# Kernel optimization log

Hardware: AMD Instinct MI355X
Metric: run time of the kernel (lower is better)

The kernel has to match this reference:

```python
import jax, jax.numpy as jnp
import numpy as np

E, H, S, B = 256, 512, 128, 512
C_EXP = 10.0  # tanh_exploration
N_COUNT_MAX = 20
T_STEPS = 100  # (max(counts)+1)*5 upper bound, static for scan


def setup_inputs() -> dict:
    key = jax.random.key(0)
    ks = jax.random.split(key, 24)
    def rn(k, shape, scale=0.02):
        return jax.random.normal(k, shape, dtype=jnp.float32) * scale
    inv_sqrt_h = 1.0 / np.sqrt(H)
    return {
        "decoder_input": rn(ks[0], (B, E), 1.0),
        "embedded_inputs": rn(ks[1], (S, B, E), 1.0),
        "hx": rn(ks[2], (B, H), 1.0),
        "cx": rn(ks[3], (B, H), 1.0),
        "context": rn(ks[4], (S, B, H), 1.0),
        "counts": jax.random.randint(ks[5], (B,), 0, N_COUNT_MAX),
        "max_steps": T_STEPS,
        "Wi": rn(ks[6], (4 * H, E)), "bi": jnp.zeros((4 * H,), jnp.float32),
        "Wh": rn(ks[7], (4 * H, H)), "bh": jnp.zeros((4 * H,), jnp.float32),
        "gWq": rn(ks[8], (H, H)), "gbq": jnp.zeros((H,), jnp.float32),
        "gWr": rn(ks[9], (H, H)), "gbr": jnp.zeros((H,), jnp.float32),
        "gv": jax.random.uniform(ks[10], (H,), jnp.float32, -inv_sqrt_h, inv_sqrt_h),
        "pWq": rn(ks[11], (H, H)), "pbq": jnp.zeros((H,), jnp.float32),
        "pWr": rn(ks[12], (H, H)), "pbr": jnp.zeros((H,), jnp.float32),
        "pv": jax.random.uniform(ks[13], (H,), jnp.float32, -inv_sqrt_h, inv_sqrt_h),
    }


def _attn(q, context, Wq, bq, Wr, br, v):
    # q: [B,H]; context: [S,B,H]. 1x1 conv over source dim == per-position linear.
    e = jnp.einsum('sbh,oh->bos', context, Wr) + br[None, :, None]  # [B,H,S]
    qp = q @ Wq.T + bq                                             # [B,H]
    u = jnp.einsum('h,bhs->bs', v, jnp.tanh(qp[:, :, None] + e))   # [B,S]
    return e, u


def reference(decoder_input, embedded_inputs, hx, cx, context, counts, max_steps,
              Wi, bi, Wh, bh, gWq, gbq, gWr, gbr, gv, pWq, pbq, pWr, pbr, pv):
    base_key = jax.random.key(42)
    batch_idx = jnp.arange(B)

    def step(carry, t):
        hx_, cx_, dec_in, fmask, fmmask = carry
        # LSTM cell
        gates = dec_in @ Wi.T + bi + hx_ @ Wh.T + bh
        ig, fg, cg, og = jnp.split(gates, 4, axis=1)
        cy = jax.nn.sigmoid(fg) * cx_ + jax.nn.sigmoid(ig) * jnp.tanh(cg)
        hy = jax.nn.sigmoid(og) * jnp.tanh(cy)
        # one glimpse (n_glimpses=1, use_tanh=False)
        e_g, lg = _attn(hy, context, gWq, gbq, gWr, gbr, gv)
        g_l = jnp.einsum('bhs,bs->bh', e_g, jax.nn.softmax(lg, axis=-1))
        # pointer (use_tanh=True, C=10)
        _, up = _attn(g_l, context, pWq, pbq, pWr, pbr, pv)
        logits_p = C_EXP * jnp.tanh(up)
        probs = jax.nn.softmax(logits_p, axis=-1)          # [B,S]
        idxs = jax.random.categorical(jax.random.fold_in(base_key, t), logits_p)
        idxs = (idxs * fmask).astype(jnp.int32)
        probs_out = probs * (fmask * fmmask)[:, None].astype(probs.dtype)
        new_fmask = fmask * (idxs != 0).astype(jnp.int32)
        new_fmmask = jnp.where(t == counts, 0, fmmask)
        dec_next = embedded_inputs[idxs, batch_idx, :]     # [B,E]
        return (hy, cy, dec_next, new_fmask, new_fmmask), (probs_out, idxs)

    ones = jnp.ones((B,), jnp.int32)
    init = (hx, cx, decoder_input, ones, ones)
    (hx, cx, _, _, _), (probs_seq, sel) = jax.lax.scan(
        step, init, jnp.arange(max_steps))
    # match torch: per-batch stacked outputs concatenated -> [B*T, S]
    outputs = jnp.transpose(probs_seq, (1, 0, 2)).reshape(B * max_steps, S)
    return outputs, sel, hx, cx
```

## Files before the change

kernel.cpp:

```cpp
#include <hip/hip_runtime.h>
#include <stdint.h>
#include <math.h>

typedef unsigned int u32;

constexpr int kB = 512, kS = 128, kH = 512, kE = 256, kT = 100;
constexpr int kNG = 4 * kH;

constexpr size_t SZ_E = (size_t)kS * kB * kH;
constexpr size_t OFF_EG  = 0;
constexpr size_t OFF_EP  = OFF_EG + SZ_E;
constexpr size_t OFF_U   = OFF_EP + SZ_E;
constexpr size_t OFF_P   = OFF_U + (size_t)kB * kS;
constexpr size_t OFF_QP  = OFF_P + (size_t)kB * kS;
constexpr size_t OFF_GL  = OFF_QP + (size_t)kB * kH;
constexpr size_t OFF_G   = OFF_GL + (size_t)kB * kH;
constexpr size_t OFF_HX  = OFF_G + (size_t)kB * kNG;
constexpr size_t OFF_CX  = OFF_HX + (size_t)kB * kH;
constexpr size_t OFF_DC  = OFF_CX + (size_t)kB * kH;
constexpr size_t OFF_FM  = OFF_DC + (size_t)kB * kE;
constexpr size_t OFF_FMM = OFF_FM + kB;
constexpr size_t WS_FLOATS = OFF_FMM + kB;

__global__ __launch_bounds__(256) void sentinel_k(float* __restrict__ outSel, float val) {
  int i = blockIdx.x * blockDim.x + threadIdx.x;
  if (i < kT * kB) outSel[i] = val;
}

__device__ __forceinline__ u32 rotl32(u32 v, int d) { return (v << d) | (v >> (32 - d)); }

__device__ __forceinline__ void tf2x32(u32 k0, u32 k1, u32 x0, u32 x1, u32& o0, u32& o1) {
  u32 ks2 = k0 ^ k1 ^ 0x1BD11BDAu;
  x0 += k0; x1 += k1;
#define RND_(r) { x0 += x1; x1 = rotl32(x1, r); x1 ^= x0; }
  RND_(13) RND_(15) RND_(26) RND_(6)   x0 += k1;  x1 += ks2 + 1u;
  RND_(17) RND_(29) RND_(16) RND_(24)  x0 += ks2; x1 += k0 + 2u;
  RND_(13) RND_(15) RND_(26) RND_(6)   x0 += k0;  x1 += k1 + 3u;
  RND_(17) RND_(29) RND_(16) RND_(24)  x0 += k1;  x1 += ks2 + 4u;
  RND_(13) RND_(15) RND_(26) RND_(6)   x0 += ks2; x1 += k0 + 5u;
#undef RND_
  o0 = x0; o1 = x1;
}

__device__ __forceinline__ float sigf(float x) { return 1.0f / (1.0f + expf(-x)); }

__global__ __launch_bounds__(512) void precompute_e(const float* __restrict__ ctx,
                                                    const float* __restrict__ Wg,
                                                    const float* __restrict__ bg,
                                                    const float* __restrict__ Wp,
                                                    const float* __restrict__ bp,
                                                    float* __restrict__ EG,
                                                    float* __restrict__ EP) {
  __shared__ float ctxs[8][512];
  __shared__ float Wgs[512][33];
  __shared__ float Wps[512][33];
  const int tid = threadIdx.x;
  const size_t m0 = (size_t)blockIdx.x * 8;
  for (int idx = tid; idx < 8 * 512; idx += 512) {
    ctxs[idx >> 9][idx & 511] = ctx[(m0 + (idx >> 9)) * 512 + (idx & 511)];
  }
  float accg[8] = {}, accp[8] = {};
  for (int k0 = 0; k0 < 512; k0 += 32) {
    __syncthreads();
    for (int idx = tid; idx < 512 * 32; idx += 512) {
      int row = idx >> 5, kk = idx & 31;
      Wgs[row][kk] = Wg[(size_t)row * 512 + k0 + kk];
      Wps[row][kk] = Wp[(size_t)row * 512 + k0 + kk];
    }
    __syncthreads();
#pragma unroll 4
    for (int kk = 0; kk < 32; ++kk) {
      float wg = Wgs[tid][kk], wp = Wps[tid][kk];
#pragma unroll
      for (int mi = 0; mi < 8; ++mi) {
        float a = ctxs[mi][k0 + kk];
        accg[mi] = fmaf(a, wg, accg[mi]);
        accp[mi] = fmaf(a, wp, accp[mi]);
      }
    }
  }
  float bgv = bg[tid], bpv = bp[tid];
#pragma unroll
  for (int mi = 0; mi < 8; ++mi) {
    size_t m = m0 + mi;
    EG[m * 512 + tid] = accg[mi] + bgv;
    EP[m * 512 + tid] = accp[mi] + bpv;
  }
}

template <int K, int NB, bool FIRST>
__global__ __launch_bounds__(512) void gemm_v2(const float* __restrict__ A,
                                               const float* __restrict__ W,
                                               const float* __restrict__ bias,
                                               const float* __restrict__ Cin,
                                               float* __restrict__ C, int N) {
  __shared__ float As[NB][K];
  __shared__ float Ws[512][33];
  const int b0 = blockIdx.y * NB;
  const int o0 = blockIdx.x * 512;
  const int tid = threadIdx.x;
  for (int idx = tid; idx < NB * K; idx += 512) {
    int bb = idx / K, k = idx % K;
    As[bb][k] = A[(size_t)(b0 + bb) * K + k];
  }
  float acc[NB] = {};
  for (int k0 = 0; k0 < K; k0 += 32) {
    __syncthreads();
    for (int idx = tid; idx < 512 * 32; idx += 512) {
      int row = idx >> 5, kk = idx & 31;
      Ws[row][kk] = W[(size_t)(o0 + row) * K + k0 + kk];
    }
    __syncthreads();
#pragma unroll 4
    for (int kk = 0; kk < 32; ++kk) {
      float w = Ws[tid][kk];
#pragma unroll
      for (int bb = 0; bb < NB; ++bb) acc[bb] = fmaf(As[bb][k0 + kk], w, acc[bb]);
    }
  }
  float bv = bias[o0 + tid];
#pragma unroll
  for (int bb = 0; bb < NB; ++bb) {
    size_t off = (size_t)(b0 + bb) * N + o0 + tid;
    C[off] = FIRST ? (acc[bb] + bv) : ((Cin[off] + acc[bb]) + bv);
  }
}

__global__ __launch_bounds__(256) void init_k(const float* __restrict__ dec_in,
                                              const float* __restrict__ hx0,
                                              const float* __restrict__ cx0,
                                              float* __restrict__ dec, float* __restrict__ hx,
                                              float* __restrict__ cx, int* __restrict__ fm,
                                              int* __restrict__ fmm) {
  int i = blockIdx.x * blockDim.x + threadIdx.x;
  if (i < kB * kH) { hx[i] = hx0[i]; cx[i] = cx0[i]; }
  if (i < kB * kE) dec[i] = dec_in[i];
  if (i < kB) { fm[i] = 1; fmm[i] = 1; }
}

__global__ __launch_bounds__(256) void lstm_act(const float* __restrict__ gates,
                                                float* __restrict__ hx, float* __restrict__ cx) {
  int i = blockIdx.x * blockDim.x + threadIdx.x;
  int b = i >> 9, h = i & (kH - 1);
  const float* g = gates + (size_t)b * kNG;
  float ig = g[h], fg = g[h + kH], cg = g[h + 2 * kH], og = g[h + 3 * kH];
  float cyv = sigf(fg) * cx[i] + sigf(ig) * tanhf(cg);
  float hyv = sigf(og) * tanhf(cyv);
  cx[i] = cyv;
  hx[i] = hyv;
}

__global__ __launch_bounds__(512) void fused_step(
    const float* __restrict__ EG, const float* __restrict__ EP, const float* __restrict__ gWq,
    const float* __restrict__ gbq, const float* __restrict__ gv, const float* __restrict__ pWq,
    const float* __restrict__ pbq, const float* __restrict__ pv, const float* __restrict__ emb,
    const int* __restrict__ counts, float* __restrict__ HX, float* __restrict__ DC,
    int* __restrict__ fmask, int* __restrict__ fmmask, float* __restrict__ outP,
    float* __restrict__ outSel, int t) {
  __shared__ float Ws[512][33];
  __shared__ float hs[512];
  __shared__ float qs[512];
  __shared__ float gvs[512];
  __shared__ float gls[512];
  __shared__ float u[128], sL[128], ex[128], kv[128];
  __shared__ float mred, sred, sMult;
  __shared__ int sIdx;

  const int b = blockIdx.x;
  const int tid = threadIdx.x;
  const int wave = tid >> 6, lane = tid & 63;

  hs[tid] = HX[(size_t)b * kH + tid];
  gvs[tid] = gv[tid];
  __syncthreads();

  {
    float acc = 0.f;
    for (int k0 = 0; k0 < 512; k0 += 32) {
      __syncthreads();
      for (int idx = tid; idx < 512 * 32; idx += 512) {
        int row = idx >> 5, kk = idx & 31;
        Ws[row][kk] = gWq[(size_t)row * 512 + k0 + kk];
      }
      __syncthreads();
#pragma unroll 8
      for (int kk = 0; kk < 32; ++kk) acc = fmaf(hs[k0 + kk], Ws[tid][kk], acc);
    }
    qs[tid] = acc + gbq[tid];
  }
  __syncthreads();

  for (int r = 0; r < 16; ++r) {
    int s = wave + 8 * r;
    const float* row = EG + ((size_t)s * kB + b) * kH;
    float a = 0.f;
#pragma unroll
    for (int i = 0; i < 8; ++i) {
      int h = lane + 64 * i;
      a = fmaf(gvs[h], tanhf(qs[h] + row[h]), a);
    }
#pragma unroll
    for (int off = 32; off > 0; off >>= 1) a += __shfl_xor(a, off);
    if (lane == 0) u[s] = a;
  }
  __syncthreads();

  if (tid == 0) { float m = u[0]; for (int i = 1; i < 128; ++i) m = fmaxf(m, u[i]); mred = m; }
  __syncthreads();
  if (tid < 128) ex[tid] = expf(u[tid] - mred);
  __syncthreads();
  if (tid == 0) { float s = 0.f; for (int i = 0; i < 128; ++i) s += ex[i]; sred = s; }
  __syncthreads();
  if (tid < 128) ex[tid] = ex[tid] / sred;
  __syncthreads();

  {
    float acc = 0.f;
    for (int s = 0; s < 128; ++s) acc = fmaf(EG[((size_t)s * kB + b) * kH + tid], ex[s], acc);
    gls[tid] = acc;
  }
  __syncthreads();

  {
    float acc = 0.f;
    for (int k0 = 0; k0 < 512; k0 += 32) {
      __syncthreads();
      for (int idx = tid; idx < 512 * 32; idx += 512) {
        int row = idx >> 5, kk = idx & 31;
        Ws[row][kk] = pWq[(size_t)row * 512 + k0 + kk];
      }
      __syncthreads();
#pragma unroll 8
      for (int kk = 0; kk < 32; ++kk) acc = fmaf(gls[k0 + kk], Ws[tid][kk], acc);
    }
    qs[tid] = acc + pbq[tid];
    gvs[tid] = pv[tid];
  }
  __syncthreads();

  for (int r = 0; r < 16; ++r) {
    int s = wave + 8 * r;
    const float* row = EP + ((size_t)s * kB + b) * kH;
    float a = 0.f;
#pragma unroll
    for (int i = 0; i < 8; ++i) {
      int h = lane + 64 * i;
      a = fmaf(gvs[h], tanhf(qs[h] + row[h]), a);
    }
#pragma unroll
    for (int off = 32; off > 0; off >>= 1) a += __shfl_xor(a, off);
    if (lane == 0) u[s] = a;
  }
  __syncthreads();

  if (tid < 128) sL[tid] = 10.0f * tanhf(u[tid]);
  __syncthreads();
  if (tid == 0) { float m = sL[0]; for (int i = 1; i < 128; ++i) m = fmaxf(m, sL[i]); mred = m; }
  __syncthreads();
  if (tid < 128) ex[tid] = expf(sL[tid] - mred);
  __syncthreads();
  if (tid == 0) { float s = 0.f; for (int i = 0; i < 128; ++i) s += ex[i]; sred = s; }
  __syncthreads();
  if (tid < 128) {
    u32 fk0, fk1;
    tf2x32(0u, 42u, 0u, (u32)t, fk0, fk1);
    u32 j = (u32)(b * kS + tid);
    u32 y0, y1;
    tf2x32(fk0, fk1, 0u, j, y0, y1);
    u32 bits = y0 ^ y1;
    float f = __uint_as_float(0x3f800000u | (bits >> 9)) - 1.0f;
    float uu = (f > 0.0f) ? f : 1.17549435082228751e-38f;
    float z = -logf(-logf(uu));
    kv[tid] = sL[tid] + z;
  }
  __syncthreads();
  if (tid == 0) {
    float best = kv[0];
    int ia = 0;
    for (int i = 1; i < 128; ++i)
      if (kv[i] > best) { best = kv[i]; ia = i; }
    int fm = fmask[b], fmm = fmmask[b];
    int idx = ia * fm;
    outSel[(size_t)t * kB + b] = (float)idx;
    fmask[b] = (idx != 0) ? fm : 0;
    fmmask[b] = (t == counts[b]) ? 0 : fmm;
    sIdx = idx;
    sMult = (float)(fm * fmm);
  }
  __syncthreads();
  if (tid < 128) outP[((size_t)b * kT + t) * kS + tid] = (ex[tid] / sred) * sMult;
  if (tid < 256) DC[(size_t)b * kE + tid] = emb[((size_t)sIdx * kB + b) * kE + tid];
}

__global__ __launch_bounds__(256) void final_copy(const float* __restrict__ hx,
                                                  const float* __restrict__ cx,
                                                  float* __restrict__ o2, float* __restrict__ o3) {
  int i = blockIdx.x * blockDim.x + threadIdx.x;
  if (i < kB * kH) { o2[i] = hx[i]; o3[i] = cx[i]; }
}

extern "C" void kernel_launch(void* const* d_in, const int* in_sizes, int n_in, void* d_out,
                              int out_size, void* d_ws, size_t ws_size, hipStream_t stream) {
  const float* dec_in = (const float*)d_in[0];
  const float* emb = (const float*)d_in[1];
  const float* hx0 = (const float*)d_in[2];
  const float* cx0 = (const float*)d_in[3];
  const float* ctx = (const float*)d_in[4];
  const int* counts = (const int*)d_in[5];
  const float* Wi = (const float*)d_in[7];
  const float* bi = (const float*)d_in[8];
  const float* Wh = (const float*)d_in[9];
  const float* bh = (const float*)d_in[10];
  const float* gWq = (const float*)d_in[11];
  const float* gbq = (const float*)d_in[12];
  const float* gWr = (const float*)d_in[13];
  const float* gbr = (const float*)d_in[14];
  const float* gv = (const float*)d_in[15];
  const float* pWq = (const float*)d_in[16];
  const float* pbq = (const float*)d_in[17];
  const float* pWr = (const float*)d_in[18];
  const float* pbr = (const float*)d_in[19];
  const float* pv = (const float*)d_in[20];

  float* out = (float*)d_out;
  float* outP = out;
  float* outSel = out + (size_t)kB * kT * kS;
  float* outHx = outSel + (size_t)kT * kB;
  float* outCx = outHx + (size_t)kB * kH;

  if (ws_size < WS_FLOATS * sizeof(float)) {
    double wsMB = (double)ws_size / (1024.0 * 1024.0);
    if (wsMB > 80000.0) wsMB = 80000.0;
    hipLaunchKernelGGL(sentinel_k, dim3((kT * kB + 255) / 256), dim3(256), 0, stream, outSel,
                       (float)(1000.0 + wsMB));
    return;
  }

  float* base = (float*)d_ws;
  float* EG = base + OFF_EG;
  float* EP = base + OFF_EP;
  float* G  = base + OFF_G;
  float* HX = base + OFF_HX;
  float* CX = base + OFF_CX;
  float* DC = base + OFF_DC;
  int* FM  = (int*)(base + OFF_FM);
  int* FMM = (int*)(base + OFF_FMM);

  hipLaunchKernelGGL(precompute_e, dim3(kS * kB / 8), dim3(512), 0, stream, ctx, gWr, gbr, pWr,
                     pbr, EG, EP);
  hipLaunchKernelGGL(init_k, dim3(kB * kH / 256), dim3(256), 0, stream, dec_in, hx0, cx0, DC, HX,
                     CX, FM, FMM);

  for (int t = 0; t < kT; ++t) {
    hipLaunchKernelGGL((gemm_v2<256, 8, true>), dim3(4, 64), dim3(512), 0, stream, DC, Wi, bi,
                       (const float*)nullptr, G, kNG);
    hipLaunchKernelGGL((gemm_v2<512, 8, false>), dim3(4, 64), dim3(512), 0, stream, HX, Wh, bh, G,
                       G, kNG);
    hipLaunchKernelGGL(lstm_act, dim3(kB * kH / 256), dim3(256), 0, stream, G, HX, CX);
    hipLaunchKernelGGL(fused_step, dim3(kB), dim3(512), 0, stream, EG, EP, gWq, gbq, gv, pWq, pbq,
                       pv, emb, counts, HX, DC, FM, FMM, outP, outSel, t);
  }
  hipLaunchKernelGGL(final_copy, dim3(kB * kH / 256), dim3(256), 0, stream, HX, CX, outHx, outCx);
}
```

Baseline: 36.14 ms.

## Replace per-block query matvecs with batched GEMMs and split fused step kernel

The glimpse and pointer query projections were computed inside the per-batch fused kernel, with every block re-streaming the full HxH weight matrix through shared memory. These projections now run as batched GEMM launches that share the weights across batch rows. The fused kernel is split into an attention/glimpse kernel and a pointer/sampling kernel that read the precomputed projections from workspace. This trades redundant weight traffic for extra kernel launches and global round trips of the intermediate vectors.

```diff
diff --git a/kernel.cpp b/kernel.cpp
--- a/kernel.cpp
+++ b/kernel.cpp
@@ -150,44 +150,19 @@
   hx[i] = hyv;
 }
 
-__global__ __launch_bounds__(512) void fused_step(
-    const float* __restrict__ EG, const float* __restrict__ EP, const float* __restrict__ gWq,
-    const float* __restrict__ gbq, const float* __restrict__ gv, const float* __restrict__ pWq,
-    const float* __restrict__ pbq, const float* __restrict__ pv, const float* __restrict__ emb,
-    const int* __restrict__ counts, float* __restrict__ HX, float* __restrict__ DC,
-    int* __restrict__ fmask, int* __restrict__ fmmask, float* __restrict__ outP,
-    float* __restrict__ outSel, int t) {
-  __shared__ float Ws[512][33];
-  __shared__ float hs[512];
-  __shared__ float qs[512];
-  __shared__ float gvs[512];
-  __shared__ float gls[512];
-  __shared__ float u[128], sL[128], ex[128], kv[128];
-  __shared__ float mred, sred, sMult;
-  __shared__ int sIdx;
-
+__global__ __launch_bounds__(512) void fused_A(const float* __restrict__ EG,
+                                               const float* __restrict__ qp,
+                                               const float* __restrict__ gv,
+                                               float* __restrict__ GL) {
+  __shared__ float qs[512], gvs[512], gls_unused[1];
+  __shared__ float u[128], ps[128];
+  __shared__ float mred, sred;
   const int b = blockIdx.x;
   const int tid = threadIdx.x;
   const int wave = tid >> 6, lane = tid & 63;
 
-  hs[tid] = HX[(size_t)b * kH + tid];
+  qs[tid] = qp[(size_t)b * kH + tid];
   gvs[tid] = gv[tid];
-  __syncthreads();
-
-  {
-    float acc = 0.f;
-    for (int k0 = 0; k0 < 512; k0 += 32) {
-      __syncthreads();
-      for (int idx = tid; idx < 512 * 32; idx += 512) {
-        int row = idx >> 5, kk = idx & 31;
-        Ws[row][kk] = gWq[(size_t)row * 512 + k0 + kk];
-      }
-      __syncthreads();
-#pragma unroll 8
-      for (int kk = 0; kk < 32; ++kk) acc = fmaf(hs[k0 + kk], Ws[tid][kk], acc);
-    }
-    qs[tid] = acc + gbq[tid];
-  }
   __syncthreads();
 
   for (int r = 0; r < 16; ++r) {
@@ -207,35 +182,37 @@
 
   if (tid == 0) { float m = u[0]; for (int i = 1; i < 128; ++i) m = fmaxf(m, u[i]); mred = m; }
   __syncthreads();
-  if (tid < 128) ex[tid] = expf(u[tid] - mred);
-  __syncthreads();
-  if (tid == 0) { float s = 0.f; for (int i = 0; i < 128; ++i) s += ex[i]; sred = s; }
-  __syncthreads();
-  if (tid < 128) ex[tid] = ex[tid] / sred;
-  __syncthreads();
-
-  {
-    float acc = 0.f;
-    for (int s = 0; s < 128; ++s) acc = fmaf(EG[((size_t)s * kB + b) * kH + tid], ex[s], acc);
-    gls[tid] = acc;
-  }
-  __syncthreads();
-
-  {
-    float acc = 0.f;
-    for (int k0 = 0; k0 < 512; k0 += 32) {
-      __syncthreads();
-      for (int idx = tid; idx < 512 * 32; idx += 512) {
-        int row = idx >> 5, kk = idx & 31;
-        Ws[row][kk] = pWq[(size_t)row * 512 + k0 + kk];
-      }
-      __syncthreads();
-#pragma unroll 8
-      for (int kk = 0; kk < 32; ++kk) acc = fmaf(gls[k0 + kk], Ws[tid][kk], acc);
-    }
-    qs[tid] = acc + pbq[tid];
-    gvs[tid] = pv[tid];
-  }
+  if (tid < 128) ps[tid] = expf(u[tid] - mred);
+  __syncthreads();
+  if (tid == 0) { float s = 0.f; for (int i = 0; i < 128; ++i) s += ps[i]; sred = s; }
+  __syncthreads();
+  if (tid < 128) ps[tid] = ps[tid] / sred;
+  __syncthreads();
+
+  float acc = 0.f;
+  for (int s = 0; s < 128; ++s) acc = fmaf(EG[((size_t)s * kB + b) * kH + tid], ps[s], acc);
+  GL[(size_t)b * kH + tid] = acc;
+  (void)gls_unused;
+}
+
+__global__ __launch_bounds__(512) void fused_B(const float* __restrict__ EP,
+                                               const float* __restrict__ qp,
+                                               const float* __restrict__ pv,
+                                               const float* __restrict__ emb,
+                                               const int* __restrict__ counts,
+                                               float* __restrict__ DC, int* __restrict__ fmask,
+                                               int* __restrict__ fmmask, float* __restrict__ outP,
+                                               float* __restrict__ outSel, int t) {
+  __shared__ float qs[512], gvs[512];
+  __shared__ float u[128], sL[128], ex[128], kv[128];
+  __shared__ float mred, sred, sMult;
+  __shared__ int sIdx;
+  const int b = blockIdx.x;
+  const int tid = threadIdx.x;
+  const int wave = tid >> 6, lane = tid & 63;
+
+  qs[tid] = qp[(size_t)b * kH + tid];
+  gvs[tid] = pv[tid];
   __syncthreads();
 
   for (int r = 0; r < 16; ++r) {
@@ -339,6 +316,8 @@
   float* base = (float*)d_ws;
   float* EG = base + OFF_EG;
   float* EP = base + OFF_EP;
+  float* QP = base + OFF_QP;
+  float* GL = base + OFF_GL;
   float* G  = base + OFF_G;
   float* HX = base + OFF_HX;
   float* CX = base + OFF_CX;
@@ -357,8 +336,13 @@
     hipLaunchKernelGGL((gemm_v2<512, 8, false>), dim3(4, 64), dim3(512), 0, stream, HX, Wh, bh, G,
                        G, kNG);
     hipLaunchKernelGGL(lstm_act, dim3(kB * kH / 256), dim3(256), 0, stream, G, HX, CX);
-    hipLaunchKernelGGL(fused_step, dim3(kB), dim3(512), 0, stream, EG, EP, gWq, gbq, gv, pWq, pbq,
-                       pv, emb, counts, HX, DC, FM, FMM, outP, outSel, t);
+    hipLaunchKernelGGL((gemm_v2<512, 4, true>), dim3(1, 128), dim3(512), 0, stream, HX, gWq, gbq,
+                       (const float*)nullptr, QP, kH);
+    hipLaunchKernelGGL(fused_A, dim3(kB), dim3(512), 0, stream, EG, QP, gv, GL);
+    hipLaunchKernelGGL((gemm_v2<512, 4, true>), dim3(1, 128), dim3(512), 0, stream, GL, pWq, pbq,
+                       (const float*)nullptr, QP, kH);
+    hipLaunchKernelGGL(fused_B, dim3(kB), dim3(512), 0, stream, EP, QP, pv, emb, counts, DC, FM,
+                       FMM, outP, outSel, t);
   }
   hipLaunchKernelGGL(final_copy, dim3(kB * kH / 256), dim3(256), 0, stream, HX, CX, outHx, outCx);
 }
```

Result: slower. 41.06 ms (+13.6%).

## Replace per-step kernel launches with a persistent cooperative megakernel using grid syncs

Applied to the files above, without the earlier changes.

Replaces the 400 per-timestep launches (two gate GEMMs, LSTM activation, fused attention step) with one cooperative persistent kernel of 512 blocks that loops over all 100 steps, separated by grid.sync barriers. The LSTM gate GEMM is fused with the activation. The query projections for glimpse and pointer are now computed once per 8-batch tile instead of once per batch row, which cuts redundant weight loads. The cost is five grid-wide barriers per step and phases where only 64 or 256 of the 512 blocks do work. If the cooperative launch fails, the old multi-kernel path runs instead.

```diff
diff --git a/kernel.cpp b/kernel.cpp
--- a/kernel.cpp
+++ b/kernel.cpp
@@ -1,7 +1,9 @@
 #include <hip/hip_runtime.h>
+#include <hip/hip_cooperative_groups.h>
 #include <stdint.h>
 #include <math.h>
 
+namespace cg = cooperative_groups;
 typedef unsigned int u32;
 
 constexpr int kB = 512, kS = 128, kH = 512, kE = 256, kT = 100;
@@ -85,6 +87,256 @@
     size_t m = m0 + mi;
     EG[m * 512 + tid] = accg[mi] + bgv;
     EP[m * 512 + tid] = accp[mi] + bpv;
+  }
+}
+
+__global__ __launch_bounds__(512, 4) void mega_k(
+    const float* __restrict__ EG, const float* __restrict__ EP, const float* __restrict__ Wi,
+    const float* __restrict__ bi, const float* __restrict__ Wh, const float* __restrict__ bh,
+    const float* __restrict__ gWq, const float* __restrict__ gbq, const float* __restrict__ gv,
+    const float* __restrict__ pWq, const float* __restrict__ pbq, const float* __restrict__ pv,
+    const float* __restrict__ emb, const int* __restrict__ counts,
+    const float* __restrict__ dec_in, const float* __restrict__ hx0,
+    const float* __restrict__ cx0, float* __restrict__ HX, float* __restrict__ CX,
+    float* __restrict__ DC, float* __restrict__ QP, float* __restrict__ GL, int* __restrict__ FM,
+    int* __restrict__ FMM, float* __restrict__ outP, float* __restrict__ outSel,
+    float* __restrict__ outHx, float* __restrict__ outCx) {
+  cg::grid_group grid = cg::this_grid();
+  __shared__ float Ws[512][33];
+  __shared__ float As[8][32];
+  __shared__ float qs[512], gvs[512];
+  __shared__ float u[128], ps[128], sL[128], kv[128];
+  __shared__ float mred, sred, sMult;
+  __shared__ int sIdx;
+
+  const int bid = blockIdx.x;
+  const int tid = threadIdx.x;
+  const int wave = tid >> 6, lane = tid & 63;
+
+  {
+    int i = bid * 512 + tid;
+    HX[i] = hx0[i];
+    CX[i] = cx0[i];
+    if (i < kB * kE) DC[i] = dec_in[i];
+    if (i < kB) { FM[i] = 1; FMM[i] = 1; }
+  }
+  grid.sync();
+
+  for (int t = 0; t < kT; ++t) {
+    if (bid < 256) {
+      const int h0 = (bid & 3) * 128;
+      const int b0 = (bid >> 2) * 8;
+      const int hl = tid & 127, bs = tid >> 7;
+      float aI[2][4] = {}, aH[2][4] = {};
+      for (int k0 = 0; k0 < 768; k0 += 32) {
+        const bool isI = (k0 < 256);
+        __syncthreads();
+        if (tid < 256) {
+          int bb = tid >> 5, kk = tid & 31;
+          int k = k0 + kk;
+          As[bb][kk] = isI ? DC[(size_t)(b0 + bb) * kE + k]
+                           : HX[(size_t)(b0 + bb) * kH + (k - 256)];
+        }
+        for (int idx = tid; idx < 512 * 32; idx += 512) {
+          int r = idx >> 5, kk = idx & 31;
+          int grow = ((r >> 7) << 9) + h0 + (r & 127);
+          int k = k0 + kk;
+          Ws[r][kk] = isI ? Wi[(size_t)grow * kE + k] : Wh[(size_t)grow * kH + (k - 256)];
+        }
+        __syncthreads();
+        if (isI) {
+#pragma unroll 4
+          for (int kk = 0; kk < 32; ++kk) {
+            float a0 = As[bs][kk], a1 = As[bs + 4][kk];
+#pragma unroll
+            for (int g = 0; g < 4; ++g) {
+              float w = Ws[g * 128 + hl][kk];
+              aI[0][g] = fmaf(a0, w, aI[0][g]);
+              aI[1][g] = fmaf(a1, w, aI[1][g]);
+            }
+          }
+        } else {
+#pragma unroll 4
+          for (int kk = 0; kk < 32; ++kk) {
+            float a0 = As[bs][kk], a1 = As[bs + 4][kk];
+#pragma unroll
+            for (int g = 0; g < 4; ++g) {
+              float w = Ws[g * 128 + hl][kk];
+              aH[0][g] = fmaf(a0, w, aH[0][g]);
+              aH[1][g] = fmaf(a1, w, aH[1][g]);
+            }
+          }
+        }
+      }
+      const int h = h0 + hl;
+#pragma unroll
+      for (int i = 0; i < 2; ++i) {
+        int b = b0 + bs + i * 4;
+        float ig = ((aI[i][0] + bi[h]) + aH[i][0]) + bh[h];
+        float fg = ((aI[i][1] + bi[512 + h]) + aH[i][1]) + bh[512 + h];
+        float cgv = ((aI[i][2] + bi[1024 + h]) + aH[i][2]) + bh[1024 + h];
+        float og = ((aI[i][3] + bi[1536 + h]) + aH[i][3]) + bh[1536 + h];
+        size_t off = (size_t)b * kH + h;
+        float cyv = sigf(fg) * CX[off] + sigf(ig) * tanhf(cgv);
+        float hyv = sigf(og) * tanhf(cyv);
+        CX[off] = cyv;
+        HX[off] = hyv;
+      }
+    }
+    grid.sync();
+
+    if (bid < 64) {
+      const int b0 = bid * 8;
+      float acc[8] = {};
+      for (int k0 = 0; k0 < 512; k0 += 32) {
+        __syncthreads();
+        if (tid < 256) {
+          int bb = tid >> 5, kk = tid & 31;
+          As[bb][kk] = HX[(size_t)(b0 + bb) * kH + k0 + kk];
+        }
+        for (int idx = tid; idx < 512 * 32; idx += 512) {
+          int r = idx >> 5, kk = idx & 31;
+          Ws[r][kk] = gWq[(size_t)r * 512 + k0 + kk];
+        }
+        __syncthreads();
+#pragma unroll 4
+        for (int kk = 0; kk < 32; ++kk) {
+          float w = Ws[tid][kk];
+#pragma unroll
+          for (int bb = 0; bb < 8; ++bb) acc[bb] = fmaf(As[bb][kk], w, acc[bb]);
+        }
+      }
+      float bv = gbq[tid];
+#pragma unroll
+      for (int bb = 0; bb < 8; ++bb) QP[(size_t)(b0 + bb) * kH + tid] = acc[bb] + bv;
+    }
+    grid.sync();
+
+    {
+      const int b = bid;
+      qs[tid] = QP[(size_t)b * kH + tid];
+      gvs[tid] = gv[tid];
+      __syncthreads();
+      for (int r = 0; r < 16; ++r) {
+        int s = wave + 8 * r;
+        const float* row = EG + ((size_t)s * kB + b) * kH;
+        float a = 0.f;
+#pragma unroll
+        for (int i = 0; i < 8; ++i) {
+          int h = lane + 64 * i;
+          a = fmaf(gvs[h], tanhf(qs[h] + row[h]), a);
+        }
+#pragma unroll
+        for (int off = 32; off > 0; off >>= 1) a += __shfl_xor(a, off);
+        if (lane == 0) u[s] = a;
+      }
+      __syncthreads();
+      if (tid == 0) { float m = u[0]; for (int i = 1; i < 128; ++i) m = fmaxf(m, u[i]); mred = m; }
+      __syncthreads();
+      if (tid < 128) ps[tid] = expf(u[tid] - mred);
+      __syncthreads();
+      if (tid == 0) { float s2 = 0.f; for (int i = 0; i < 128; ++i) s2 += ps[i]; sred = s2; }
+      __syncthreads();
+      if (tid < 128) ps[tid] = ps[tid] / sred;
+      __syncthreads();
+      float acc = 0.f;
+#pragma unroll 4
+      for (int s = 0; s < 128; ++s) acc = fmaf(EG[((size_t)s * kB + b) * kH + tid], ps[s], acc);
+      GL[(size_t)b * kH + tid] = acc;
+    }
+    grid.sync();
+
+    if (bid < 64) {
+      const int b0 = bid * 8;
+      float acc[8] = {};
+      for (int k0 = 0; k0 < 512; k0 += 32) {
+        __syncthreads();
+        if (tid < 256) {
+          int bb = tid >> 5, kk = tid & 31;
+          As[bb][kk] = GL[(size_t)(b0 + bb) * kH + k0 + kk];
+        }
+        for (int idx = tid; idx < 512 * 32; idx += 512) {
+          int r = idx >> 5, kk = idx & 31;
+          Ws[r][kk] = pWq[(size_t)r * 512 + k0 + kk];
+        }
+        __syncthreads();
+#pragma unroll 4
+        for (int kk = 0; kk < 32; ++kk) {
+          float w = Ws[tid][kk];
+#pragma unroll
+          for (int bb = 0; bb < 8; ++bb) acc[bb] = fmaf(As[bb][kk], w, acc[bb]);
+        }
+      }
+      float bv = pbq[tid];
+#pragma unroll
+      for (int bb = 0; bb < 8; ++bb) QP[(size_t)(b0 + bb) * kH + tid] = acc[bb] + bv;
+    }
+    grid.sync();
+
+    {
+      const int b = bid;
+      qs[tid] = QP[(size_t)b * kH + tid];
+      gvs[tid] = pv[tid];
+      __syncthreads();
+      for (int r = 0; r < 16; ++r) {
+        int s = wave + 8 * r;
+        const float* row = EP + ((size_t)s * kB + b) * kH;
+        float a = 0.f;
+#pragma unroll
+        for (int i = 0; i < 8; ++i) {
+          int h = lane + 64 * i;
+          a = fmaf(gvs[h], tanhf(qs[h] + row[h]), a);
+        }
+#pragma unroll
+        for (int off = 32; off > 0; off >>= 1) a += __shfl_xor(a, off);
+        if (lane == 0) u[s] = a;
+      }
+      __syncthreads();
+      if (tid < 128) sL[tid] = 10.0f * tanhf(u[tid]);
+      __syncthreads();
+      if (tid == 0) { float m = sL[0]; for (int i = 1; i < 128; ++i) m = fmaxf(m, sL[i]); mred = m; }
+      __syncthreads();
+      if (tid < 128) ps[tid] = expf(sL[tid] - mred);
+      __syncthreads();
+      if (tid == 0) { float s2 = 0.f; for (int i = 0; i < 128; ++i) s2 += ps[i]; sred = s2; }
+      __syncthreads();
+      if (tid < 128) {
+        u32 fk0, fk1;
+        tf2x32(0u, 42u, 0u, (u32)t, fk0, fk1);
+        u32 j = (u32)(b * kS + tid);
+        u32 y0, y1;
+        tf2x32(fk0, fk1, 0u, j, y0, y1);
+        u32 bits = y0 ^ y1;
+        float f = __uint_as_float(0x3f800000u | (bits >> 9)) - 1.0f;
+        float uu = (f > 0.0f) ? f : 1.17549435082228751e-38f;
+        float z = -logf(-logf(uu));
+        kv[tid] = sL[tid] + z;
+      }
+      __syncthreads();
+      if (tid == 0) {
+        float best = kv[0];
+        int ia = 0;
+        for (int i = 1; i < 128; ++i)
+          if (kv[i] > best) { best = kv[i]; ia = i; }
+        int fm = FM[b], fmm = FMM[b];
+        int idx = ia * fm;
+        outSel[(size_t)t * kB + b] = (float)idx;
+        FM[b] = (idx != 0) ? fm : 0;
+        FMM[b] = (t == counts[b]) ? 0 : fmm;
+        sIdx = idx;
+        sMult = (float)(fm * fmm);
+      }
+      __syncthreads();
+      if (tid < 128) outP[((size_t)b * kT + t) * kS + tid] = (ps[tid] / sred) * sMult;
+      if (tid < 256) DC[(size_t)b * kE + tid] = emb[((size_t)sIdx * kB + b) * kE + tid];
+    }
+    grid.sync();
+  }
+
+  {
+    int i = bid * 512 + tid;
+    outHx[i] = HX[i];
+    outCx[i] = CX[i];
   }
 }
 
@@ -173,7 +425,6 @@
   hs[tid] = HX[(size_t)b * kH + tid];
   gvs[tid] = gv[tid];
   __syncthreads();
-
   {
     float acc = 0.f;
     for (int k0 = 0; k0 < 512; k0 += 32) {
@@ -189,7 +440,6 @@
     qs[tid] = acc + gbq[tid];
   }
   __syncthreads();
-
   for (int r = 0; r < 16; ++r) {
     int s = wave + 8 * r;
     const float* row = EG + ((size_t)s * kB + b) * kH;
@@ -204,7 +454,6 @@
     if (lane == 0) u[s] = a;
   }
   __syncthreads();
-
   if (tid == 0) { float m = u[0]; for (int i = 1; i < 128; ++i) m = fmaxf(m, u[i]); mred = m; }
   __syncthreads();
   if (tid < 128) ex[tid] = expf(u[tid] - mred);
@@ -213,14 +462,12 @@
   __syncthreads();
   if (tid < 128) ex[tid] = ex[tid] / sred;
   __syncthreads();
-
   {
     float acc = 0.f;
     for (int s = 0; s < 128; ++s) acc = fmaf(EG[((size_t)s * kB + b) * kH + tid], ex[s], acc);
     gls[tid] = acc;
   }
   __syncthreads();
-
   {
     float acc = 0.f;
     for (int k0 = 0; k0 < 512; k0 += 32) {
@@ -237,7 +484,6 @@
     gvs[tid] = pv[tid];
   }
   __syncthreads();
-
   for (int r = 0; r < 16; ++r) {
     int s = wave + 8 * r;
     const float* row = EP + ((size_t)s * kB + b) * kH;
@@ -252,7 +498,6 @@
     if (lane == 0) u[s] = a;
   }
   __syncthreads();
-
   if (tid < 128) sL[tid] = 10.0f * tanhf(u[tid]);
   __syncthreads();
   if (tid == 0) { float m = sL[0]; for (int i = 1; i < 128; ++i) m = fmaxf(m, sL[i]); mred = m; }
@@ -339,6 +584,8 @@
   float* base = (float*)d_ws;
   float* EG = base + OFF_EG;
   float* EP = base + OFF_EP;
+  float* QP = base + OFF_QP;
+  float* GL = base + OFF_GL;
   float* G  = base + OFF_G;
   float* HX = base + OFF_HX;
   float* CX = base + OFF_CX;
@@ -348,9 +595,19 @@
 
   hipLaunchKernelGGL(precompute_e, dim3(kS * kB / 8), dim3(512), 0, stream, ctx, gWr, gbr, pWr,
                      pbr, EG, EP);
+
+  void* args[] = {(void*)&EG,  (void*)&EP,  (void*)&Wi,  (void*)&bi,   (void*)&Wh,
+                  (void*)&bh,  (void*)&gWq, (void*)&gbq, (void*)&gv,   (void*)&pWq,
+                  (void*)&pbq, (void*)&pv,  (void*)&emb, (void*)&counts, (void*)&dec_in,
+                  (void*)&hx0, (void*)&cx0, (void*)&HX,  (void*)&CX,   (void*)&DC,
+                  (void*)&QP,  (void*)&GL,  (void*)&FM,  (void*)&FMM,  (void*)&outP,
+                  (void*)&outSel, (void*)&outHx, (void*)&outCx};
+  hipError_t st = hipLaunchCooperativeKernel((const void*)mega_k, dim3(512), dim3(512), args, 0,
+                                             stream);
+  if (st == hipSuccess) return;
+
   hipLaunchKernelGGL(init_k, dim3(kB * kH / 256), dim3(256), 0, stream, dec_in, hx0, cx0, DC, HX,
                      CX, FM, FMM);
-
   for (int t = 0; t < kT; ++t) {
     hipLaunchKernelGGL((gemm_v2<256, 8, true>), dim3(4, 64), dim3(512), 0, stream, DC, Wi, bi,
                        (const float*)nullptr, G, kNG);
```

New measurement: 91.61 ms. 2.53x slower.

## Fuse all decode steps into one persistent per-batch kernel with transposed weights

Applied to the files above, without the earlier changes.

Replaces the per-step launches of two gate GEMMs, the LSTM activation and the attention step with a single persistent kernel. Each block owns one batch row and keeps h, c, the decoder input and the mask flags in shared memory for all 100 steps. The LSTM, glimpse and pointer weights are transposed once up front so every thread reads them as coalesced row vectors straight from global memory. This removes roughly 400 kernel launches and the global round-trips of the intermediate state. The cost is that every block now re-reads the full LSTM weight matrices each step instead of sharing them across 8 batch rows, which multiplies weight traffic through the cache hierarchy.

```diff
diff --git a/kernel.cpp b/kernel.cpp
--- a/kernel.cpp
+++ b/kernel.cpp
@@ -5,22 +5,15 @@
 typedef unsigned int u32;
 
 constexpr int kB = 512, kS = 128, kH = 512, kE = 256, kT = 100;
-constexpr int kNG = 4 * kH;
 
 constexpr size_t SZ_E = (size_t)kS * kB * kH;
 constexpr size_t OFF_EG  = 0;
 constexpr size_t OFF_EP  = OFF_EG + SZ_E;
-constexpr size_t OFF_U   = OFF_EP + SZ_E;
-constexpr size_t OFF_P   = OFF_U + (size_t)kB * kS;
-constexpr size_t OFF_QP  = OFF_P + (size_t)kB * kS;
-constexpr size_t OFF_GL  = OFF_QP + (size_t)kB * kH;
-constexpr size_t OFF_G   = OFF_GL + (size_t)kB * kH;
-constexpr size_t OFF_HX  = OFF_G + (size_t)kB * kNG;
-constexpr size_t OFF_CX  = OFF_HX + (size_t)kB * kH;
-constexpr size_t OFF_DC  = OFF_CX + (size_t)kB * kH;
-constexpr size_t OFF_FM  = OFF_DC + (size_t)kB * kE;
-constexpr size_t OFF_FMM = OFF_FM + kB;
-constexpr size_t WS_FLOATS = OFF_FMM + kB;
+constexpr size_t OFF_WIT = OFF_EP + SZ_E;
+constexpr size_t OFF_WHT = OFF_WIT + (size_t)kE * 2048;
+constexpr size_t OFF_GQT = OFF_WHT + (size_t)kH * 2048;
+constexpr size_t OFF_PQT = OFF_GQT + (size_t)kH * kH;
+constexpr size_t WS_FLOATS = OFF_PQT + (size_t)kH * kH;
 
 __global__ __launch_bounds__(256) void sentinel_k(float* __restrict__ outSel, float val) {
   int i = blockIdx.x * blockDim.x + threadIdx.x;
@@ -88,215 +81,185 @@
   }
 }
 
-template <int K, int NB, bool FIRST>
-__global__ __launch_bounds__(512) void gemm_v2(const float* __restrict__ A,
-                                               const float* __restrict__ W,
-                                               const float* __restrict__ bias,
-                                               const float* __restrict__ Cin,
-                                               float* __restrict__ C, int N) {
-  __shared__ float As[NB][K];
-  __shared__ float Ws[512][33];
-  const int b0 = blockIdx.y * NB;
-  const int o0 = blockIdx.x * 512;
-  const int tid = threadIdx.x;
-  for (int idx = tid; idx < NB * K; idx += 512) {
-    int bb = idx / K, k = idx % K;
-    As[bb][k] = A[(size_t)(b0 + bb) * K + k];
-  }
-  float acc[NB] = {};
-  for (int k0 = 0; k0 < K; k0 += 32) {
-    __syncthreads();
-    for (int idx = tid; idx < 512 * 32; idx += 512) {
-      int row = idx >> 5, kk = idx & 31;
-      Ws[row][kk] = W[(size_t)(o0 + row) * K + k0 + kk];
-    }
-    __syncthreads();
-#pragma unroll 4
-    for (int kk = 0; kk < 32; ++kk) {
-      float w = Ws[tid][kk];
-#pragma unroll
-      for (int bb = 0; bb < NB; ++bb) acc[bb] = fmaf(As[bb][k0 + kk], w, acc[bb]);
-    }
-  }
-  float bv = bias[o0 + tid];
-#pragma unroll
-  for (int bb = 0; bb < NB; ++bb) {
-    size_t off = (size_t)(b0 + bb) * N + o0 + tid;
-    C[off] = FIRST ? (acc[bb] + bv) : ((Cin[off] + acc[bb]) + bv);
-  }
-}
-
-__global__ __launch_bounds__(256) void init_k(const float* __restrict__ dec_in,
-                                              const float* __restrict__ hx0,
-                                              const float* __restrict__ cx0,
-                                              float* __restrict__ dec, float* __restrict__ hx,
-                                              float* __restrict__ cx, int* __restrict__ fm,
-                                              int* __restrict__ fmm) {
-  int i = blockIdx.x * blockDim.x + threadIdx.x;
-  if (i < kB * kH) { hx[i] = hx0[i]; cx[i] = cx0[i]; }
-  if (i < kB * kE) dec[i] = dec_in[i];
-  if (i < kB) { fm[i] = 1; fmm[i] = 1; }
-}
-
-__global__ __launch_bounds__(256) void lstm_act(const float* __restrict__ gates,
-                                                float* __restrict__ hx, float* __restrict__ cx) {
-  int i = blockIdx.x * blockDim.x + threadIdx.x;
-  int b = i >> 9, h = i & (kH - 1);
-  const float* g = gates + (size_t)b * kNG;
-  float ig = g[h], fg = g[h + kH], cg = g[h + 2 * kH], og = g[h + 3 * kH];
-  float cyv = sigf(fg) * cx[i] + sigf(ig) * tanhf(cg);
-  float hyv = sigf(og) * tanhf(cyv);
-  cx[i] = cyv;
-  hx[i] = hyv;
-}
-
-__global__ __launch_bounds__(512) void fused_step(
-    const float* __restrict__ EG, const float* __restrict__ EP, const float* __restrict__ gWq,
-    const float* __restrict__ gbq, const float* __restrict__ gv, const float* __restrict__ pWq,
-    const float* __restrict__ pbq, const float* __restrict__ pv, const float* __restrict__ emb,
-    const int* __restrict__ counts, float* __restrict__ HX, float* __restrict__ DC,
-    int* __restrict__ fmask, int* __restrict__ fmmask, float* __restrict__ outP,
-    float* __restrict__ outSel, int t) {
-  __shared__ float Ws[512][33];
-  __shared__ float hs[512];
-  __shared__ float qs[512];
-  __shared__ float gvs[512];
-  __shared__ float gls[512];
+__global__ __launch_bounds__(256) void transpose_k(const float* __restrict__ in,
+                                                   float* __restrict__ out, int O, int K) {
+  int flat = blockIdx.x * 256 + threadIdx.x;
+  if (flat < O * K) {
+    int o = flat % O, k = flat / O;
+    out[flat] = in[(size_t)o * K + k];
+  }
+}
+
+__global__ __launch_bounds__(512) void persist_k(
+    const float* __restrict__ EG, const float* __restrict__ EP, const float* __restrict__ WiT,
+    const float* __restrict__ WhT, const float* __restrict__ bi, const float* __restrict__ bh,
+    const float* __restrict__ gQT, const float* __restrict__ gbq, const float* __restrict__ gv,
+    const float* __restrict__ pQT, const float* __restrict__ pbq, const float* __restrict__ pv,
+    const float* __restrict__ emb, const int* __restrict__ counts,
+    const float* __restrict__ dec_in, const float* __restrict__ hx0,
+    const float* __restrict__ cx0, float* __restrict__ outP, float* __restrict__ outSel,
+    float* __restrict__ outHx, float* __restrict__ outCx) {
+  __shared__ float hs[512], cs[512], dec[256], qs[512], gls[512];
+  __shared__ float gvs[512], pvs[512];
   __shared__ float u[128], sL[128], ex[128], kv[128];
   __shared__ float mred, sred, sMult;
-  __shared__ int sIdx;
+  __shared__ int sIdx, sFM, sFMM;
 
   const int b = blockIdx.x;
   const int tid = threadIdx.x;
   const int wave = tid >> 6, lane = tid & 63;
 
-  hs[tid] = HX[(size_t)b * kH + tid];
+  hs[tid] = hx0[(size_t)b * kH + tid];
+  cs[tid] = cx0[(size_t)b * kH + tid];
+  if (tid < kE) dec[tid] = dec_in[(size_t)b * kE + tid];
   gvs[tid] = gv[tid];
+  pvs[tid] = pv[tid];
+  if (tid == 0) { sFM = 1; sFMM = 1; }
+  const int cnt = counts[b];
+  const float biR0 = bi[tid], biR1 = bi[512 + tid], biR2 = bi[1024 + tid], biR3 = bi[1536 + tid];
+  const float bhR0 = bh[tid], bhR1 = bh[512 + tid], bhR2 = bh[1024 + tid], bhR3 = bh[1536 + tid];
+  const float gbqR = gbq[tid], pbqR = pbq[tid];
   __syncthreads();
 
-  {
-    float acc = 0.f;
-    for (int k0 = 0; k0 < 512; k0 += 32) {
-      __syncthreads();
-      for (int idx = tid; idx < 512 * 32; idx += 512) {
-        int row = idx >> 5, kk = idx & 31;
-        Ws[row][kk] = gWq[(size_t)row * 512 + k0 + kk];
+  for (int t = 0; t < kT; ++t) {
+    float aI0 = 0.f, aI1 = 0.f, aI2 = 0.f, aI3 = 0.f;
+#pragma unroll 4
+    for (int k = 0; k < kE; ++k) {
+      float a = dec[k];
+      const float* wr = WiT + (size_t)k * 2048 + tid;
+      aI0 = fmaf(a, wr[0], aI0);
+      aI1 = fmaf(a, wr[512], aI1);
+      aI2 = fmaf(a, wr[1024], aI2);
+      aI3 = fmaf(a, wr[1536], aI3);
+    }
+    float aH0 = 0.f, aH1 = 0.f, aH2 = 0.f, aH3 = 0.f;
+#pragma unroll 4
+    for (int k = 0; k < kH; ++k) {
+      float a = hs[k];
+      const float* wr = WhT + (size_t)k * 2048 + tid;
+      aH0 = fmaf(a, wr[0], aH0);
+      aH1 = fmaf(a, wr[512], aH1);
+      aH2 = fmaf(a, wr[1024], aH2);
+      aH3 = fmaf(a, wr[1536], aH3);
+    }
+    float ig = ((aI0 + biR0) + aH0) + bhR0;
+    float fg = ((aI1 + biR1) + aH1) + bhR1;
+    float cgv = ((aI2 + biR2) + aH2) + bhR2;
+    float og = ((aI3 + biR3) + aH3) + bhR3;
+    float cyv = sigf(fg) * cs[tid] + sigf(ig) * tanhf(cgv);
+    float hyv = sigf(og) * tanhf(cyv);
+    __syncthreads();
+    cs[tid] = cyv;
+    hs[tid] = hyv;
+    __syncthreads();
+
+    {
+      float acc = 0.f;
+#pragma unroll 8
+      for (int k = 0; k < kH; ++k) acc = fmaf(hs[k], gQT[(size_t)k * kH + tid], acc);
+      qs[tid] = acc + gbqR;
+    }
+    __syncthreads();
+
+#pragma unroll 2
+    for (int r = 0; r < 16; ++r) {
+      int s = wave + 8 * r;
+      const float* row = EG + ((size_t)s * kB + b) * kH;
+      float a = 0.f;
+#pragma unroll
+      for (int i = 0; i < 8; ++i) {
+        int h = lane + 64 * i;
+        a = fmaf(gvs[h], tanhf(qs[h] + row[h]), a);
       }
-      __syncthreads();
+#pragma unroll
+      for (int off = 32; off > 0; off >>= 1) a += __shfl_xor(a, off);
+      if (lane == 0) u[s] = a;
+    }
+    __syncthreads();
+
+    if (tid == 0) { float m = u[0]; for (int i = 1; i < 128; ++i) m = fmaxf(m, u[i]); mred = m; }
+    __syncthreads();
+    if (tid < 128) ex[tid] = expf(u[tid] - mred);
+    __syncthreads();
+    if (tid == 0) { float s = 0.f; for (int i = 0; i < 128; ++i) s += ex[i]; sred = s; }
+    __syncthreads();
+    if (tid < 128) ex[tid] = ex[tid] / sred;
+    __syncthreads();
+
+    {
+      float acc = 0.f;
+#pragma unroll 4
+      for (int s = 0; s < 128; ++s) acc = fmaf(EG[((size_t)s * kB + b) * kH + tid], ex[s], acc);
+      gls[tid] = acc;
+    }
+    __syncthreads();
+
+    {
+      float acc = 0.f;
 #pragma unroll 8
-      for (int kk = 0; kk < 32; ++kk) acc = fmaf(hs[k0 + kk], Ws[tid][kk], acc);
-    }
-    qs[tid] = acc + gbq[tid];
-  }
-  __syncthreads();
-
-  for (int r = 0; r < 16; ++r) {
-    int s = wave + 8 * r;
-    const float* row = EG + ((size_t)s * kB + b) * kH;
-    float a = 0.f;
-#pragma unroll
-    for (int i = 0; i < 8; ++i) {
-      int h = lane + 64 * i;
-      a = fmaf(gvs[h], tanhf(qs[h] + row[h]), a);
-    }
-#pragma unroll
-    for (int off = 32; off > 0; off >>= 1) a += __shfl_xor(a, off);
-    if (lane == 0) u[s] = a;
-  }
-  __syncthreads();
-
-  if (tid == 0) { float m = u[0]; for (int i = 1; i < 128; ++i) m = fmaxf(m, u[i]); mred = m; }
-  __syncthreads();
-  if (tid < 128) ex[tid] = expf(u[tid] - mred);
-  __syncthreads();
-  if (tid == 0) { float s = 0.f; for (int i = 0; i < 128; ++i) s += ex[i]; sred = s; }
-  __syncthreads();
-  if (tid < 128) ex[tid] = ex[tid] / sred;
-  __syncthreads();
-
-  {
-    float acc = 0.f;
-    for (int s = 0; s < 128; ++s) acc = fmaf(EG[((size_t)s * kB + b) * kH + tid], ex[s], acc);
-    gls[tid] = acc;
-  }
-  __syncthreads();
-
-  {
-    float acc = 0.f;
-    for (int k0 = 0; k0 < 512; k0 += 32) {
-      __syncthreads();
-      for (int idx = tid; idx < 512 * 32; idx += 512) {
-        int row = idx >> 5, kk = idx & 31;
-        Ws[row][kk] = pWq[(size_t)row * 512 + k0 + kk];
+      for (int k = 0; k < kH; ++k) acc = fmaf(gls[k], pQT[(size_t)k * kH + tid], acc);
+      qs[tid] = acc + pbqR;
+    }
+    __syncthreads();
+
+#pragma unroll 2
+    for (int r = 0; r < 16; ++r) {
+      int s = wave + 8 * r;
+      const float* row = EP + ((size_t)s * kB + b) * kH;
+      float a = 0.f;
+#pragma unroll
+      for (int i = 0; i < 8; ++i) {
+        int h = lane + 64 * i;
+        a = fmaf(pvs[h], tanhf(qs[h] + row[h]), a);
       }
-      __syncthreads();
-#pragma unroll 8
-      for (int kk = 0; kk < 32; ++kk) acc = fmaf(gls[k0 + kk], Ws[tid][kk], acc);
-    }
-    qs[tid] = acc + pbq[tid];
-    gvs[tid] = pv[tid];
-  }
-  __syncthreads();
-
-  for (int r = 0; r < 16; ++r) {
-    int s = wave + 8 * r;
-    const float* row = EP + ((size_t)s * kB + b) * kH;
-    float a = 0.f;
-#pragma unroll
-    for (int i = 0; i < 8; ++i) {
-      int h = lane + 64 * i;
-      a = fmaf(gvs[h], tanhf(qs[h] + row[h]), a);
-    }
-#pragma unroll
-    for (int off = 32; off > 0; off >>= 1) a += __shfl_xor(a, off);
-    if (lane == 0) u[s] = a;
-  }
-  __syncthreads();
-
-  if (tid < 128) sL[tid] = 10.0f * tanhf(u[tid]);
-  __syncthreads();
-  if (tid == 0) { float m = sL[0]; for (int i = 1; i < 128; ++i) m = fmaxf(m, sL[i]); mred = m; }
-  __syncthreads();
-  if (tid < 128) ex[tid] = expf(sL[tid] - mred);
-  __syncthreads();
-  if (tid == 0) { float s = 0.f; for (int i = 0; i < 128; ++i) s += ex[i]; sred = s; }
-  __syncthreads();
-  if (tid < 128) {
-    u32 fk0, fk1;
-    tf2x32(0u, 42u, 0u, (u32)t, fk0, fk1);
-    u32 j = (u32)(b * kS + tid);
-    u32 y0, y1;
-    tf2x32(fk0, fk1, 0u, j, y0, y1);
-    u32 bits = y0 ^ y1;
-    float f = __uint_as_float(0x3f800000u | (bits >> 9)) - 1.0f;
-    float uu = (f > 0.0f) ? f : 1.17549435082228751e-38f;
-    float z = -logf(-logf(uu));
-    kv[tid] = sL[tid] + z;
-  }
-  __syncthreads();
-  if (tid == 0) {
-    float best = kv[0];
-    int ia = 0;
-    for (int i = 1; i < 128; ++i)
-      if (kv[i] > best) { best = kv[i]; ia = i; }
-    int fm = fmask[b], fmm = fmmask[b];
-    int idx = ia * fm;
-    outSel[(size_t)t * kB + b] = (float)idx;
-    fmask[b] = (idx != 0) ? fm : 0;
-    fmmask[b] = (t == counts[b]) ? 0 : fmm;
-    sIdx = idx;
-    sMult = (float)(fm * fmm);
-  }
-  __syncthreads();
-  if (tid < 128) outP[((size_t)b * kT + t) * kS + tid] = (ex[tid] / sred) * sMult;
-  if (tid < 256) DC[(size_t)b * kE + tid] = emb[((size_t)sIdx * kB + b) * kE + tid];
-}
-
-__global__ __launch_bounds__(256) void final_copy(const float* __restrict__ hx,
-                                                  const float* __restrict__ cx,
-                                                  float* __restrict__ o2, float* __restrict__ o3) {
-  int i = blockIdx.x * blockDim.x + threadIdx.x;
-  if (i < kB * kH) { o2[i] = hx[i]; o3[i] = cx[i]; }
+#pragma unroll
+      for (int off = 32; off > 0; off >>= 1) a += __shfl_xor(a, off);
+      if (lane == 0) u[s] = a;
+    }
+    __syncthreads();
+
+    if (tid < 128) sL[tid] = 10.0f * tanhf(u[tid]);
+    __syncthreads();
+    if (tid == 0) { float m = sL[0]; for (int i = 1; i < 128; ++i) m = fmaxf(m, sL[i]); mred = m; }
+    __syncthreads();
+    if (tid < 128) ex[tid] = expf(sL[tid] - mred);
+    __syncthreads();
+    if (tid == 0) { float s = 0.f; for (int i = 0; i < 128; ++i) s += ex[i]; sred = s; }
+    __syncthreads();
+    if (tid < 128) {
+      u32 fk0, fk1;
+      tf2x32(0u, 42u, 0u, (u32)t, fk0, fk1);
+      u32 j = (u32)(b * kS + tid);
+      u32 y0, y1;
+      tf2x32(fk0, fk1, 0u, j, y0, y1);
+      u32 bits = y0 ^ y1;
+      float f = __uint_as_float(0x3f800000u | (bits >> 9)) - 1.0f;
+      float uu = (f > 0.0f) ? f : 1.17549435082228751e-38f;
+      float z = -logf(-logf(uu));
+      kv[tid] = sL[tid] + z;
+    }
+    __syncthreads();
+    if (tid == 0) {
+      float best = kv[0];
+      int ia = 0;
+      for (int i = 1; i < 128; ++i)
+        if (kv[i] > best) { best = kv[i]; ia = i; }
+      int fm = sFM, fmm = sFMM;
+      int idx = ia * fm;
+      outSel[(size_t)t * kB + b] = (float)idx;
+      sFM = (idx != 0) ? fm : 0;
+      sFMM = (t == cnt) ? 0 : fmm;
+      sIdx = idx;
+      sMult = (float)(fm * fmm);
+    }
+    __syncthreads();
+    if (tid < 128) outP[((size_t)b * kT + t) * kS + tid] = (ex[tid] / sred) * sMult;
+    if (tid < kE) dec[tid] = emb[((size_t)sIdx * kB + b) * kE + tid];
+    __syncthreads();
+  }
+
+  outHx[(size_t)b * kH + tid] = hs[tid];
+  outCx[(size_t)b * kH + tid] = cs[tid];
 }
 
 extern "C" void kernel_launch(void* const* d_in, const int* in_sizes, int n_in, void* d_out,
@@ -337,28 +300,25 @@
   }
 
   float* base = (float*)d_ws;
-  float* EG = base + OFF_EG;
-  float* EP = base + OFF_EP;
-  float* G  = base + OFF_G;
-  float* HX = base + OFF_HX;
-  float* CX = base + OFF_CX;
-  float* DC = base + OFF_DC;
-  int* FM  = (int*)(base + OFF_FM);
-  int* FMM = (int*)(base + OFF_FMM);
+  float* EG  = base + OFF_EG;
+  float* EP  = base + OFF_EP;
+  float* WiT = base + OFF_WIT;
+  float* WhT = base + OFF_WHT;
+  float* GQT = base + OFF_GQT;
+  float* PQT = base + OFF_PQT;
 
   hipLaunchKernelGGL(precompute_e, dim3(kS * kB / 8), dim3(512), 0, stream, ctx, gWr, gbr, pWr,
                      pbr, EG, EP);
-  hipLaunchKernelGGL(init_k, dim3(kB * kH / 256), dim3(256), 0, stream, dec_in, hx0, cx0, DC, HX,
-                     CX, FM, FMM);
-
-  for (int t = 0; t < kT; ++t) {
-    hipLaunchKernelGGL((gemm_v2<256, 8, true>), dim3(4, 64), dim3(512), 0, stream, DC, Wi, bi,
-                       (const float*)nullptr, G, kNG);
-    hipLaunchKernelGGL((gemm_v2<512, 8, false>), dim3(4, 64), dim3(512), 0, stream, HX, Wh, bh, G,
-                       G, kNG);
-    hipLaunchKernelGGL(lstm_act, dim3(kB * kH / 256), dim3(256), 0, stream, G, HX, CX);
-    hipLaunchKernelGGL(fused_step, dim3(kB), dim3(512), 0, stream, EG, EP, gWq, gbq, gv, pWq, pbq,
-                       pv, emb, counts, HX, DC, FM, FMM, outP, outSel, t);
-  }
-  hipLaunchKernelGGL(final_copy, dim3(kB * kH / 256), dim3(256), 0, stream, HX, CX, outHx, outCx);
-}
+  hipLaunchKernelGGL(transpose_k, dim3((2048 * kE + 255) / 256), dim3(256), 0, stream, Wi, WiT,
+                     2048, kE);
+  hipLaunchKernelGGL(transpose_k, dim3((2048 * kH + 255) / 256), dim3(256), 0, stream, Wh, WhT,
+                     2048, kH);
+  hipLaunchKernelGGL(transpose_k, dim3((kH * kH + 255) / 256), dim3(256), 0, stream, gWq, GQT, kH,
+                     kH);
+  hipLaunchKernelGGL(transpose_k, dim3((kH * kH + 255) / 256), dim3(256), 0, stream, pWq, PQT, kH,
+                     kH);
+
+  hipLaunchKernelGGL(persist_k, dim3(kB), dim3(512), 0, stream, EG, EP, WiT, WhT, bi, bh, GQT,
+                     gbq, gv, PQT, pbq, pv, emb, counts, dec_in, hx0, cx0, outP, outSel, outHx,
+                     outCx);
+}
```

Result: faster. 31.09 ms (-14.0%).
